# Optimization experiments

Measured on AMD Instinct MI355X. Metric: run time of the kernel, lower is better.

## Reference

```python
import jax, jax.numpy as jnp
import numpy as np

N = 50000      # nodes
E = 800000     # edges
IN = 64        # in_channels (also edge_dim)
H = 4          # heads
C = 64         # out_channels per head
SLOPE = 0.2    # PyG GATConv leaky_relu negative_slope
EPS = 1e-16    # PyG softmax eps


def setup_inputs() -> dict:
    key = jax.random.key(0)
    ks = jax.random.split(key, 9)
    s = 1.0 / np.sqrt(IN)
    return {
        "x": jax.random.normal(ks[0], (N, IN), jnp.float32),
        "edge_index": jax.random.randint(ks[1], (2, E), 0, N, jnp.int64),
        "edge_attr": jax.random.normal(ks[2], (E, IN), jnp.float32),
        "W": jax.random.normal(ks[3], (IN, H * C), jnp.float32) * s,
        "W_e": jax.random.normal(ks[4], (IN, H * C), jnp.float32) * s,
        "att_src": jax.random.normal(ks[5], (H, C), jnp.float32) * s,
        "att_dst": jax.random.normal(ks[6], (H, C), jnp.float32) * s,
        "att_edge": jax.random.normal(ks[7], (H, C), jnp.float32) * s,
        "bias": jnp.zeros((H * C,), jnp.float32),
    }


def reference(x, edge_index, edge_attr, W, W_e, att_src, att_dst, att_edge, bias):
    src, dst = edge_index[0], edge_index[1]
    n = x.shape[0]

    # --- add self loops with fill_value='mean' (mean of incoming edge_attr) ---
    deg = jax.ops.segment_sum(jnp.ones((src.shape[0],), x.dtype), dst, num_segments=n)
    loop_attr = jax.ops.segment_sum(edge_attr, dst, num_segments=n) / jnp.maximum(deg, 1.0)[:, None]
    loops = jnp.arange(n, dtype=src.dtype)
    src_f = jnp.concatenate([src, loops])          # [E+N]
    dst_f = jnp.concatenate([dst, loops])          # [E+N]
    ea = jnp.concatenate([edge_attr, loop_attr], axis=0)  # [E+N, IN]

    # --- node / edge projections ---
    h = (x @ W).reshape(n, H, C)                   # [N,H,C]
    a_src = jnp.einsum('nhc,hc->nh', h, att_src)   # [N,H]
    a_dst = jnp.einsum('nhc,hc->nh', h, att_dst)   # [N,H]
    he = (ea @ W_e).reshape(-1, H, C)              # [E+N,H,C]
    a_edge = jnp.einsum('ehc,hc->eh', he, att_edge)

    # --- attention logits + segment softmax over destination nodes ---
    logits = a_src[src_f] + a_dst[dst_f] + a_edge  # [E+N,H]
    logits = jax.nn.leaky_relu(logits, SLOPE)
    m = jax.ops.segment_max(logits, dst_f, num_segments=n)         # every node has a self loop
    e = jnp.exp(logits - m[dst_f])
    z = jax.ops.segment_sum(e, dst_f, num_segments=n)
    alpha = e / (z[dst_f] + EPS)                   # [E+N,H]

    # --- scatter-aggregate messages ---
    msg = h[src_f] * alpha[:, :, None]             # [E+N,H,C]
    out = jax.ops.segment_sum(msg, dst_f, num_segments=n)          # [N,H,C]
    return out.reshape(n, H * C) + bias            # concat heads
```

## Files before the change

kernel.cpp:

```cpp
#include <hip/hip_runtime.h>
#include <hip/hip_bf16.h>
#include <math.h>

#define N_NODES 50000
#define N_EDGES 800000
#define HC      256
#define SLOPE   0.2f

typedef __bf16 bf16x8 __attribute__((ext_vector_type(8)));
typedef float  f32x4  __attribute__((ext_vector_type(4)));

__device__ __forceinline__ unsigned short f2bf(float f) {
    unsigned u = __float_as_uint(f);
    unsigned r = (u + 0x7fffu + ((u >> 16) & 1u)) >> 16;
    return (unsigned short)r;
}

__device__ __forceinline__ float rlane_f(float v, int j) {
    return __uint_as_float((unsigned)__builtin_amdgcn_readlane((int)__float_as_uint(v), j));
}

__global__ __launch_bounds__(256) void k_proj(const float* __restrict__ x,
                                              const float* __restrict__ W,
                                              const float* __restrict__ att_src,
                                              const float* __restrict__ att_dst,
                                              const float* __restrict__ W_e,
                                              const float* __restrict__ att_edge,
                                              const int* __restrict__ ei,
                                              unsigned short* __restrict__ h_bf,
                                              float* __restrict__ a_src,
                                              float* __restrict__ a_dst,
                                              float* __restrict__ v_t,
                                              int* __restrict__ counts,
                                              int* __restrict__ rank) {
    if (blockIdx.x == 0) {
        int tt = threadIdx.x;
        int k = tt >> 2, jj = tt & 3;
        float s = 0.f;
        #pragma unroll
        for (int c = 0; c < 64; ++c)
            s += W_e[k * HC + jj * 64 + c] * att_edge[jj * 64 + c];
        v_t[jj * 64 + k] = s;
    }
    for (int e = blockIdx.x * 256 + threadIdx.x; e < N_EDGES;
         e += gridDim.x * 256) {
        int d = ei[N_EDGES + e];
        rank[e] = atomicAdd(&counts[d], 1);
    }

    __shared__ unsigned short hs[64 * 256];
    int t = threadIdx.x;
    int lane = t & 63;
    int w = t >> 6;
    int l15 = lane & 15;
    int quad = lane >> 4;
    int row0 = blockIdx.x * 64;

    bf16x8 bh[8], bl[8];
    #pragma unroll
    for (int ct = 0; ct < 4; ++ct) {
        #pragma unroll
        for (int ks = 0; ks < 2; ++ks) {
            bf16x8 h8, l8;
            #pragma unroll
            for (int j = 0; j < 8; ++j) {
                float f = W[(ks * 32 + quad * 8 + j) * 256 + w * 64 + ct * 16 + l15];
                __bf16 hi = (__bf16)f;
                h8[j] = hi;
                l8[j] = (__bf16)(f - (float)hi);
            }
            bh[ct * 2 + ks] = h8;
            bl[ct * 2 + ks] = l8;
        }
    }
    float att_s[4], att_d[4];
    #pragma unroll
    for (int ct = 0; ct < 4; ++ct) {
        att_s[ct] = att_src[w * 64 + ct * 16 + l15];
        att_d[ct] = att_dst[w * 64 + ct * 16 + l15];
    }

    #pragma unroll
    for (int rt = 0; rt < 4; ++rt) {
        int row_a = row0 + rt * 16 + l15;
        if (row_a >= N_NODES) row_a = N_NODES - 1;
        bf16x8 ah[2], al[2];
        #pragma unroll
        for (int ks = 0; ks < 2; ++ks) {
            const float* xp = x + (size_t)row_a * 64 + ks * 32 + quad * 8;
            float4 x0 = ((const float4*)xp)[0];
            float4 x1 = ((const float4*)xp)[1];
            float xf[8] = {x0.x, x0.y, x0.z, x0.w, x1.x, x1.y, x1.z, x1.w};
            bf16x8 h8, l8;
            #pragma unroll
            for (int j = 0; j < 8; ++j) {
                __bf16 hi = (__bf16)xf[j];
                h8[j] = hi;
                l8[j] = (__bf16)(xf[j] - (float)hi);
            }
            ah[ks] = h8;
            al[ks] = l8;
        }
        f32x4 acc[4];
        #pragma unroll
        for (int ct = 0; ct < 4; ++ct) {
            f32x4 a = {0.f, 0.f, 0.f, 0.f};
            a = __builtin_amdgcn_mfma_f32_16x16x32_bf16(ah[0], bh[ct*2+0], a, 0, 0, 0);
            a = __builtin_amdgcn_mfma_f32_16x16x32_bf16(ah[1], bh[ct*2+1], a, 0, 0, 0);
            a = __builtin_amdgcn_mfma_f32_16x16x32_bf16(ah[0], bl[ct*2+0], a, 0, 0, 0);
            a = __builtin_amdgcn_mfma_f32_16x16x32_bf16(ah[1], bl[ct*2+1], a, 0, 0, 0);
            a = __builtin_amdgcn_mfma_f32_16x16x32_bf16(al[0], bh[ct*2+0], a, 0, 0, 0);
            a = __builtin_amdgcn_mfma_f32_16x16x32_bf16(al[1], bh[ct*2+1], a, 0, 0, 0);
            acc[ct] = a;
        }
        #pragma unroll
        for (int ct = 0; ct < 4; ++ct) {
            #pragma unroll
            for (int reg = 0; reg < 4; ++reg) {
                int r = rt * 16 + quad * 4 + reg;
                hs[r * 256 + (ct * 16 + l15) * 4 + w] = f2bf(acc[ct][reg]);
            }
        }
        #pragma unroll
        for (int reg = 0; reg < 4; ++reg) {
            float ps = 0.f, pd = 0.f;
            #pragma unroll
            for (int ct = 0; ct < 4; ++ct) {
                ps += acc[ct][reg] * att_s[ct];
                pd += acc[ct][reg] * att_d[ct];
            }
            #pragma unroll
            for (int off = 1; off < 16; off <<= 1) {
                ps += __shfl_xor(ps, off);
                pd += __shfl_xor(pd, off);
            }
            int row = row0 + rt * 16 + quad * 4 + reg;
            if (l15 == 0 && row < N_NODES) {
                a_src[row * 4 + w] = ps;
                a_dst[row * 4 + w] = pd;
            }
        }
    }
    __syncthreads();
    const uint4* ls = (const uint4*)hs;
    uint4* gd = (uint4*)h_bf;
    #pragma unroll
    for (int i = 0; i < 8; ++i) {
        int g = i * 256 + t;
        int rl = g >> 5;
        if (row0 + rl < N_NODES)
            gd[(size_t)row0 * 32 + g] = ls[g];
    }
}

__global__ __launch_bounds__(1024) void k_scan(const int* __restrict__ cnt,
                                               int* __restrict__ rowptr) {
    __shared__ int wsum[16];
    int t = threadIdx.x, lane = t & 63, w = t >> 6;
    const int WR = (N_NODES + 15) / 16;
    int begin = w * WR;
    int end = begin + WR; if (end > N_NODES) end = N_NODES;
    int s = 0;
    for (int i = begin + lane; i < end; i += 64) s += cnt[i];
    #pragma unroll
    for (int off = 32; off >= 1; off >>= 1) s += __shfl_xor(s, off);
    if (lane == 0) wsum[w] = s;
    __syncthreads();
    if (t < 16) {
        int orig = wsum[t];
        int v = orig;
        #pragma unroll
        for (int off = 1; off < 16; off <<= 1) {
            int u = __shfl_up(v, off);
            if (t >= off) v += u;
        }
        wsum[t] = v - orig;
    }
    __syncthreads();
    int run = wsum[w];
    int nwin = (end - begin + 63) / 64;
    for (int win = 0; win < nwin; ++win) {
        int i = begin + win * 64 + lane;
        int c = (i < end) ? cnt[i] : 0;
        int v = c;
        #pragma unroll
        for (int off = 1; off < 64; off <<= 1) {
            int u = __shfl_up(v, off);
            if (lane >= off) v += u;
        }
        int excl = run + v - c;
        if (i < end) rowptr[i] = excl;
        run += __shfl(v, 63);
    }
    if (t == 0) rowptr[N_NODES] = N_EDGES;
}

__global__ __launch_bounds__(256) void k_edge(const int* __restrict__ ei,
                                              const float* __restrict__ edge_attr,
                                              const float* __restrict__ v_t,
                                              const int* __restrict__ rowptr,
                                              const int* __restrict__ rank,
                                              int* __restrict__ ssrc,
                                              float4* __restrict__ sl4) {
    int t = threadIdx.x;
    int lane = t & 63;
    int sub = lane & 15;
    int eq = lane >> 4;
    float4 v0 = ((const float4*)(v_t +   0))[sub];
    float4 v1 = ((const float4*)(v_t +  64))[sub];
    float4 v2 = ((const float4*)(v_t + 128))[sub];
    float4 v3 = ((const float4*)(v_t + 192))[sub];
    int wave_id = blockIdx.x * 4 + (t >> 6);
    int nwaves = gridDim.x * 4;
    const float4* ea4 = (const float4*)edge_attr;
    for (int g = wave_id; g < N_EDGES / 4; g += nwaves) {
        int e = g * 4 + eq;
        float4 ea = ea4[(size_t)e * 16 + sub];
        float p0 = ea.x * v0.x + ea.y * v0.y + ea.z * v0.z + ea.w * v0.w;
        float p1 = ea.x * v1.x + ea.y * v1.y + ea.z * v1.z + ea.w * v1.w;
        float p2 = ea.x * v2.x + ea.y * v2.y + ea.z * v2.z + ea.w * v2.w;
        float p3 = ea.x * v3.x + ea.y * v3.y + ea.z * v3.z + ea.w * v3.w;
        #pragma unroll
        for (int off = 1; off < 16; off <<= 1) {
            p0 += __shfl_xor(p0, off);
            p1 += __shfl_xor(p1, off);
            p2 += __shfl_xor(p2, off);
            p3 += __shfl_xor(p3, off);
        }
        if (sub == 0) {
            int dst = ei[N_EDGES + e];
            int src = ei[e];
            int p = rowptr[dst] + rank[e];
            ssrc[p] = src;
            sl4[p] = make_float4(p0, p1, p2, p3);
        }
    }
}

__global__ __launch_bounds__(256) void k_gather(const int* __restrict__ rowptr,
                                                const int* __restrict__ ssrc,
                                                const float4* __restrict__ sl4,
                                                const unsigned short* __restrict__ h_bf,
                                                const float* __restrict__ a_src,
                                                const float* __restrict__ a_dst,
                                                const float* __restrict__ bias,
                                                float* __restrict__ out) {
    int wave = (int)((blockIdx.x * 256u + threadIdx.x) >> 6);
    int lane = threadIdx.x & 63;
    if (wave >= N_NODES) return;
    int n = wave;
    int r0 = rowptr[n];
    int r1 = rowptr[n + 1];
    float4 ad = ((const float4*)a_dst)[n];
    const uint2* h2 = (const uint2*)h_bf;
    float a0 = 0.f, a1 = 0.f, a2 = 0.f, a3 = 0.f;
    float z0 = 0.f, z1 = 0.f, z2 = 0.f, z3 = 0.f;
    float s0 = 0.f, s1 = 0.f, s2 = 0.f, s3 = 0.f;
    for (int base = r0; base < r1; base += 64) {
        int cnt = r1 - base; if (cnt > 64) cnt = 64;
        int idx = base + (lane < cnt ? lane : 0);
        int msrc = ssrc[idx];
        float4 ae = sl4[idx];
        float4 asv = ((const float4*)a_src)[msrc];
        float l0 = ae.x + asv.x + ad.x, l1 = ae.y + asv.y + ad.y;
        float l2 = ae.z + asv.z + ad.z, l3 = ae.w + asv.w + ad.w;
        l0 = fmaxf(l0, SLOPE * l0); l1 = fmaxf(l1, SLOPE * l1);
        l2 = fmaxf(l2, SLOPE * l2); l3 = fmaxf(l3, SLOPE * l3);
        float mw0 = __expf(l0), mw1 = __expf(l1);
        float mw2 = __expf(l2), mw3 = __expf(l3);
        if (lane < cnt) {
            z0 += mw0; z1 += mw1; z2 += mw2; z3 += mw3;
            s0 += ae.x; s1 += ae.y; s2 += ae.z; s3 += ae.w;
        }
        #pragma unroll 8
        for (int j = 0; j < cnt; ++j) {
            int src = __builtin_amdgcn_readlane(msrc, j);
            float e0 = rlane_f(mw0, j), e1 = rlane_f(mw1, j);
            float e2 = rlane_f(mw2, j), e3 = rlane_f(mw3, j);
            const uint2* hp = h2 + ((size_t)(unsigned)src << 6);
            uint2 hv = hp[lane];
            float h0 = __uint_as_float(hv.x << 16);
            float h1 = __uint_as_float(hv.x & 0xffff0000u);
            float h2f = __uint_as_float(hv.y << 16);
            float h3 = __uint_as_float(hv.y & 0xffff0000u);
            a0 += h0 * e0; a1 += h1 * e1; a2 += h2f * e2; a3 += h3 * e3;
        }
    }
    #pragma unroll
    for (int off = 32; off >= 1; off >>= 1) {
        z0 += __shfl_xor(z0, off); z1 += __shfl_xor(z1, off);
        z2 += __shfl_xor(z2, off); z3 += __shfl_xor(z3, off);
        s0 += __shfl_xor(s0, off); s1 += __shfl_xor(s1, off);
        s2 += __shfl_xor(s2, off); s3 += __shfl_xor(s3, off);
    }
    float d = (float)(r1 - r0); if (d < 1.f) d = 1.f;
    float rdeg = 1.f / d;
    float4 la = ((const float4*)a_src)[n];
    float l0 = la.x + ad.x + s0 * rdeg;
    float l1 = la.y + ad.y + s1 * rdeg;
    float l2 = la.z + ad.z + s2 * rdeg;
    float l3 = la.w + ad.w + s3 * rdeg;
    l0 = fmaxf(l0, SLOPE * l0); l1 = fmaxf(l1, SLOPE * l1);
    l2 = fmaxf(l2, SLOPE * l2); l3 = fmaxf(l3, SLOPE * l3);
    float w0 = __expf(l0), w1 = __expf(l1), w2 = __expf(l2), w3 = __expf(l3);
    uint2 hv = h2[(size_t)n * 64 + lane];
    float h0 = __uint_as_float(hv.x << 16);
    float h1 = __uint_as_float(hv.x & 0xffff0000u);
    float h2f = __uint_as_float(hv.y << 16);
    float h3 = __uint_as_float(hv.y & 0xffff0000u);
    a0 += h0 * w0; z0 += w0;
    a1 += h1 * w1; z1 += w1;
    a2 += h2f * w2; z2 += w2;
    a3 += h3 * w3; z3 += w3;
    size_t ob = (size_t)n * HC + lane;
    out[ob]       = a0 / (z0 + 1e-16f) + bias[lane];
    out[ob + 64]  = a1 / (z1 + 1e-16f) + bias[64 + lane];
    out[ob + 128] = a2 / (z2 + 1e-16f) + bias[128 + lane];
    out[ob + 192] = a3 / (z3 + 1e-16f) + bias[192 + lane];
}

extern "C" void kernel_launch(void* const* d_in, const int* in_sizes, int n_in,
                              void* d_out, int out_size, void* d_ws, size_t ws_size,
                              hipStream_t stream) {
    const float* x        = (const float*)d_in[0];
    const int*   ei       = (const int*)d_in[1];
    const float* edge_attr= (const float*)d_in[2];
    const float* W        = (const float*)d_in[3];
    const float* W_e      = (const float*)d_in[4];
    const float* att_src  = (const float*)d_in[5];
    const float* att_dst  = (const float*)d_in[6];
    const float* att_edge = (const float*)d_in[7];
    const float* bias     = (const float*)d_in[8];
    float* out = (float*)d_out;

    unsigned short* h_bf  = (unsigned short*)d_ws;
    float*  a_src     = (float*)(h_bf + (size_t)N_NODES * 256);
    float*  a_dst     = a_src + N_NODES * 4;
    float*  v_t       = a_dst + N_NODES * 4;
    float4* sl4       = (float4*)(v_t + 256);
    int*    ssrc      = (int*)(sl4 + N_EDGES);
    int*    rank      = ssrc + N_EDGES;
    int*    rowptr    = rank + N_EDGES;
    int*    cnt       = rowptr + N_NODES + 1;

    hipMemsetAsync(cnt, 0, (size_t)N_NODES * sizeof(int), stream);

    k_proj<<<(N_NODES + 63) / 64, 256, 0, stream>>>(x, W, att_src, att_dst,
                                                    W_e, att_edge, ei,
                                                    h_bf, a_src, a_dst, v_t,
                                                    cnt, rank);
    k_scan<<<1, 1024, 0, stream>>>(cnt, rowptr);
    k_edge<<<2048, 256, 0, stream>>>(ei, edge_attr, v_t, rowptr, rank,
                                     ssrc, sl4);
    k_gather<<<(N_NODES + 3) / 4, 256, 0, stream>>>(rowptr, ssrc, sl4,
                                                    h_bf, a_src, a_dst,
                                                    bias, out);
}
```

Before: 496.3 us.

## Fuse edge logit projection into gather kernel via sorted edge ids

```diff
diff --git a/kernel.cpp b/kernel.cpp
--- a/kernel.cpp
+++ b/kernel.cpp
@@ -195,56 +195,33 @@
     if (t == 0) rowptr[N_NODES] = N_EDGES;
 }
 
-__global__ __launch_bounds__(256) void k_edge(const int* __restrict__ ei,
-                                              const float* __restrict__ edge_attr,
-                                              const float* __restrict__ v_t,
-                                              const int* __restrict__ rowptr,
-                                              const int* __restrict__ rank,
-                                              int* __restrict__ ssrc,
-                                              float4* __restrict__ sl4) {
-    int t = threadIdx.x;
-    int lane = t & 63;
-    int sub = lane & 15;
-    int eq = lane >> 4;
-    float4 v0 = ((const float4*)(v_t +   0))[sub];
-    float4 v1 = ((const float4*)(v_t +  64))[sub];
-    float4 v2 = ((const float4*)(v_t + 128))[sub];
-    float4 v3 = ((const float4*)(v_t + 192))[sub];
-    int wave_id = blockIdx.x * 4 + (t >> 6);
-    int nwaves = gridDim.x * 4;
-    const float4* ea4 = (const float4*)edge_attr;
-    for (int g = wave_id; g < N_EDGES / 4; g += nwaves) {
-        int e = g * 4 + eq;
-        float4 ea = ea4[(size_t)e * 16 + sub];
-        float p0 = ea.x * v0.x + ea.y * v0.y + ea.z * v0.z + ea.w * v0.w;
-        float p1 = ea.x * v1.x + ea.y * v1.y + ea.z * v1.z + ea.w * v1.w;
-        float p2 = ea.x * v2.x + ea.y * v2.y + ea.z * v2.z + ea.w * v2.w;
-        float p3 = ea.x * v3.x + ea.y * v3.y + ea.z * v3.z + ea.w * v3.w;
-        #pragma unroll
-        for (int off = 1; off < 16; off <<= 1) {
-            p0 += __shfl_xor(p0, off);
-            p1 += __shfl_xor(p1, off);
-            p2 += __shfl_xor(p2, off);
-            p3 += __shfl_xor(p3, off);
-        }
-        if (sub == 0) {
-            int dst = ei[N_EDGES + e];
-            int src = ei[e];
-            int p = rowptr[dst] + rank[e];
-            ssrc[p] = src;
-            sl4[p] = make_float4(p0, p1, p2, p3);
-        }
-    }
+__global__ __launch_bounds__(256) void k_scatter(const int* __restrict__ ei,
+                                                 const int* __restrict__ rowptr,
+                                                 const int* __restrict__ rank,
+                                                 int* __restrict__ ssrc,
+                                                 int* __restrict__ seid) {
+    int e = blockIdx.x * 256 + threadIdx.x;
+    if (e >= N_EDGES) return;
+    int dst = ei[N_EDGES + e];
+    int src = ei[e];
+    int p = rowptr[dst] + rank[e];
+    ssrc[p] = src;
+    seid[p] = e;
 }
 
 __global__ __launch_bounds__(256) void k_gather(const int* __restrict__ rowptr,
                                                 const int* __restrict__ ssrc,
-                                                const float4* __restrict__ sl4,
+                                                const int* __restrict__ seid,
+                                                const float* __restrict__ edge_attr,
+                                                const float* __restrict__ v_t,
                                                 const unsigned short* __restrict__ h_bf,
                                                 const float* __restrict__ a_src,
                                                 const float* __restrict__ a_dst,
                                                 const float* __restrict__ bias,
                                                 float* __restrict__ out) {
+    __shared__ float vts[256];
+    vts[threadIdx.x] = v_t[threadIdx.x];
+    __syncthreads();
     int wave = (int)((blockIdx.x * 256u + threadIdx.x) >> 6);
     int lane = threadIdx.x & 63;
     if (wave >= N_NODES) return;
@@ -253,6 +230,10 @@
     int r1 = rowptr[n + 1];
     float4 ad = ((const float4*)a_dst)[n];
     const uint2* h2 = (const uint2*)h_bf;
+    const float4* vt0 = (const float4*)(vts +   0);
+    const float4* vt1 = (const float4*)(vts +  64);
+    const float4* vt2 = (const float4*)(vts + 128);
+    const float4* vt3 = (const float4*)(vts + 192);
     float a0 = 0.f, a1 = 0.f, a2 = 0.f, a3 = 0.f;
     float z0 = 0.f, z1 = 0.f, z2 = 0.f, z3 = 0.f;
     float s0 = 0.f, s1 = 0.f, s2 = 0.f, s3 = 0.f;
@@ -260,17 +241,28 @@
         int cnt = r1 - base; if (cnt > 64) cnt = 64;
         int idx = base + (lane < cnt ? lane : 0);
         int msrc = ssrc[idx];
-        float4 ae = sl4[idx];
+        int eid  = seid[idx];
+        const float4* eap = (const float4*)(edge_attr + (size_t)eid * 64);
+        float ae0 = 0.f, ae1 = 0.f, ae2 = 0.f, ae3 = 0.f;
+        #pragma unroll
+        for (int c4 = 0; c4 < 16; ++c4) {
+            float4 ea = eap[c4];
+            float4 v0 = vt0[c4], v1 = vt1[c4], v2 = vt2[c4], v3 = vt3[c4];
+            ae0 += ea.x * v0.x + ea.y * v0.y + ea.z * v0.z + ea.w * v0.w;
+            ae1 += ea.x * v1.x + ea.y * v1.y + ea.z * v1.z + ea.w * v1.w;
+            ae2 += ea.x * v2.x + ea.y * v2.y + ea.z * v2.z + ea.w * v2.w;
+            ae3 += ea.x * v3.x + ea.y * v3.y + ea.z * v3.z + ea.w * v3.w;
+        }
         float4 asv = ((const float4*)a_src)[msrc];
-        float l0 = ae.x + asv.x + ad.x, l1 = ae.y + asv.y + ad.y;
-        float l2 = ae.z + asv.z + ad.z, l3 = ae.w + asv.w + ad.w;
+        float l0 = ae0 + asv.x + ad.x, l1 = ae1 + asv.y + ad.y;
+        float l2 = ae2 + asv.z + ad.z, l3 = ae3 + asv.w + ad.w;
         l0 = fmaxf(l0, SLOPE * l0); l1 = fmaxf(l1, SLOPE * l1);
         l2 = fmaxf(l2, SLOPE * l2); l3 = fmaxf(l3, SLOPE * l3);
         float mw0 = __expf(l0), mw1 = __expf(l1);
         float mw2 = __expf(l2), mw3 = __expf(l3);
         if (lane < cnt) {
             z0 += mw0; z1 += mw1; z2 += mw2; z3 += mw3;
-            s0 += ae.x; s1 += ae.y; s2 += ae.z; s3 += ae.w;
+            s0 += ae0; s1 += ae1; s2 += ae2; s3 += ae3;
         }
         #pragma unroll 8
         for (int j = 0; j < cnt; ++j) {
@@ -337,9 +329,9 @@
     float*  a_src     = (float*)(h_bf + (size_t)N_NODES * 256);
     float*  a_dst     = a_src + N_NODES * 4;
     float*  v_t       = a_dst + N_NODES * 4;
-    float4* sl4       = (float4*)(v_t + 256);
-    int*    ssrc      = (int*)(sl4 + N_EDGES);
-    int*    rank      = ssrc + N_EDGES;
+    int*    ssrc      = (int*)(v_t + 256);
+    int*    seid      = ssrc + N_EDGES;
+    int*    rank      = seid + N_EDGES;
     int*    rowptr    = rank + N_EDGES;
     int*    cnt       = rowptr + N_NODES + 1;
 
@@ -350,9 +342,10 @@
                                                     h_bf, a_src, a_dst, v_t,
                                                     cnt, rank);
     k_scan<<<1, 1024, 0, stream>>>(cnt, rowptr);
-    k_edge<<<2048, 256, 0, stream>>>(ei, edge_attr, v_t, rowptr, rank,
-                                     ssrc, sl4);
-    k_gather<<<(N_NODES + 3) / 4, 256, 0, stream>>>(rowptr, ssrc, sl4,
+    k_scatter<<<(N_EDGES + 255) / 256, 256, 0, stream>>>(ei, rowptr, rank,
+                                                         ssrc, seid);
+    k_gather<<<(N_NODES + 3) / 4, 256, 0, stream>>>(rowptr, ssrc, seid,
+                                                    edge_attr, v_t,
                                                     h_bf, a_src, a_dst,
                                                     bias, out);
 }
```

After: 924.9 us. 86.3% more time.

## Split each node's edge list across four waves per block in gather

Applied to the files above, without the earlier changes.

```diff
diff --git a/kernel.cpp b/kernel.cpp
--- a/kernel.cpp
+++ b/kernel.cpp
@@ -245,19 +245,25 @@
                                                 const float* __restrict__ a_dst,
                                                 const float* __restrict__ bias,
                                                 float* __restrict__ out) {
-    int wave = (int)((blockIdx.x * 256u + threadIdx.x) >> 6);
-    int lane = threadIdx.x & 63;
-    if (wave >= N_NODES) return;
-    int n = wave;
+    __shared__ float pa[4][4][64];
+    __shared__ float pzs[4][8];
+    int n = blockIdx.x;
+    int t = threadIdx.x;
+    int w = t >> 6;
+    int lane = t & 63;
     int r0 = rowptr[n];
     int r1 = rowptr[n + 1];
+    int deg = r1 - r0;
+    int chunk = (deg + 3) >> 2;
+    int b0 = r0 + w * chunk;
+    int b1 = b0 + chunk; if (b1 > r1) b1 = r1;
     float4 ad = ((const float4*)a_dst)[n];
     const uint2* h2 = (const uint2*)h_bf;
     float a0 = 0.f, a1 = 0.f, a2 = 0.f, a3 = 0.f;
     float z0 = 0.f, z1 = 0.f, z2 = 0.f, z3 = 0.f;
     float s0 = 0.f, s1 = 0.f, s2 = 0.f, s3 = 0.f;
-    for (int base = r0; base < r1; base += 64) {
-        int cnt = r1 - base; if (cnt > 64) cnt = 64;
+    for (int base = b0; base < b1; base += 64) {
+        int cnt = b1 - base; if (cnt > 64) cnt = 64;
         int idx = base + (lane < cnt ? lane : 0);
         int msrc = ssrc[idx];
         float4 ae = sl4[idx];
@@ -293,7 +299,27 @@
         s0 += __shfl_xor(s0, off); s1 += __shfl_xor(s1, off);
         s2 += __shfl_xor(s2, off); s3 += __shfl_xor(s3, off);
     }
-    float d = (float)(r1 - r0); if (d < 1.f) d = 1.f;
+    pa[w][0][lane] = a0; pa[w][1][lane] = a1;
+    pa[w][2][lane] = a2; pa[w][3][lane] = a3;
+    if (lane == 0) {
+        pzs[w][0] = z0; pzs[w][1] = z1; pzs[w][2] = z2; pzs[w][3] = z3;
+        pzs[w][4] = s0; pzs[w][5] = s1; pzs[w][6] = s2; pzs[w][7] = s3;
+    }
+    __syncthreads();
+    if (w != 0) return;
+    a0 = pa[0][0][lane] + pa[1][0][lane] + pa[2][0][lane] + pa[3][0][lane];
+    a1 = pa[0][1][lane] + pa[1][1][lane] + pa[2][1][lane] + pa[3][1][lane];
+    a2 = pa[0][2][lane] + pa[1][2][lane] + pa[2][2][lane] + pa[3][2][lane];
+    a3 = pa[0][3][lane] + pa[1][3][lane] + pa[2][3][lane] + pa[3][3][lane];
+    z0 = pzs[0][0] + pzs[1][0] + pzs[2][0] + pzs[3][0];
+    z1 = pzs[0][1] + pzs[1][1] + pzs[2][1] + pzs[3][1];
+    z2 = pzs[0][2] + pzs[1][2] + pzs[2][2] + pzs[3][2];
+    z3 = pzs[0][3] + pzs[1][3] + pzs[2][3] + pzs[3][3];
+    s0 = pzs[0][4] + pzs[1][4] + pzs[2][4] + pzs[3][4];
+    s1 = pzs[0][5] + pzs[1][5] + pzs[2][5] + pzs[3][5];
+    s2 = pzs[0][6] + pzs[1][6] + pzs[2][6] + pzs[3][6];
+    s3 = pzs[0][7] + pzs[1][7] + pzs[2][7] + pzs[3][7];
+    float d = (float)deg; if (d < 1.f) d = 1.f;
     float rdeg = 1.f / d;
     float4 la = ((const float4*)a_src)[n];
     float l0 = la.x + ad.x + s0 * rdeg;
@@ -352,7 +378,7 @@
     k_scan<<<1, 1024, 0, stream>>>(cnt, rowptr);
     k_edge<<<2048, 256, 0, stream>>>(ei, edge_attr, v_t, rowptr, rank,
                                      ssrc, sl4);
-    k_gather<<<(N_NODES + 3) / 4, 256, 0, stream>>>(rowptr, ssrc, sl4,
-                                                    h_bf, a_src, a_dst,
-                                                    bias, out);
-}
+    k_gather<<<N_NODES, 256, 0, stream>>>(rowptr, ssrc, sl4,
+                                          h_bf, a_src, a_dst,
+                                          bias, out);
+}
```

Result: slower. 536.5 us (+8.1%).
